# Performance work log

Measured on AMD Instinct MI355X. Metric: run time of the kernel, lower is better.

## Reference

```python
import math
import jax, jax.numpy as jnp
import numpy as np

EMBED_DIM = 512
MAX_LEN = 5000
BATCH = 16
SEQ = 4096


def _make_pe(max_len, embed_dim):
    pos = jnp.arange(max_len, dtype=jnp.float32)[:, None]
    div = jnp.exp(jnp.arange(0, embed_dim, 2, dtype=jnp.float32) * (-math.log(10000.0) / embed_dim))
    pe = jnp.zeros((max_len, embed_dim), dtype=jnp.float32)
    pe = pe.at[:, 0::2].set(jnp.sin(pos * div))
    pe = pe.at[:, 1::2].set(jnp.cos(pos * div))
    return pe[None]  # [1, max_len, embed_dim]


def setup_inputs() -> dict:
    key = jax.random.key(0)
    k1, k2 = jax.random.split(key)
    x = jax.random.normal(k1, (BATCH, SEQ, EMBED_DIM), dtype=jnp.float32)
    pe = _make_pe(MAX_LEN, EMBED_DIM)
    # RZ angles: present in the original module but provably do not affect
    # the PauliZ expectations (diagonal phases + basis-permuting CNOTs).
    param = jax.random.normal(k2, (EMBED_DIM,), dtype=jnp.float32)
    quantum_weight = jnp.full((1,), 0.5, dtype=jnp.float32)
    return {"x": x, "pe": pe, "param": param, "quantum_weight": quantum_weight}


def reference(x, pe, param, quantum_weight):
    # out = x + positional encoding
    out = x + pe[:, : x.shape[1]]  # [B, S, D]
    # Closed form of the RY(out_i)->RZ(param_i)->CNOT-chain circuit:
    #   b'_i = XOR(b_0..b_i)  =>  <Z_i> = prod_{j<=i} cos(out_j)
    # (RZ phases cancel in computational-basis probabilities; param unused.)
    quantum_out = jnp.cumprod(jnp.cos(out), axis=-1)  # [B, S, D]
    w = jax.nn.sigmoid(quantum_weight[0])
    return w * quantum_out + (1.0 - w) * out
```

## Files before the change

kernel.cpp:

```cpp
#include <hip/hip_runtime.h>

constexpr int D = 512;
constexpr int S = 4096;
constexpr int B = 16;
constexpr int ROWS = B * S;
constexpr int WAVES_PER_BLOCK = 4;

__global__ __launch_bounds__(256) void qpe_kernel(
    const float* __restrict__ x, const float* __restrict__ pe,
    const float* __restrict__ qw, float* __restrict__ out)
{
    const int lane = threadIdx.x & 63;
    const int wid  = threadIdx.x >> 6;
    const int row  = blockIdx.x * WAVES_PER_BLOCK + wid;
    const int s    = row & (S - 1);

    const float w   = 1.0f / (1.0f + __expf(-qw[0]));
    const float omw = 1.0f - w;

    const size_t base = (size_t)row * D + (size_t)lane * 8;
    const float4* xp = (const float4*)(x + base);
    const float4* pp = (const float4*)(pe + (size_t)s * D + (size_t)lane * 8);

    const float4 x0 = xp[0], x1 = xp[1];
    const float4 p0 = pp[0], p1 = pp[1];

    float o[8] = { x0.x + p0.x, x0.y + p0.y, x0.z + p0.z, x0.w + p0.w,
                   x1.x + p1.x, x1.y + p1.y, x1.z + p1.z, x1.w + p1.w };

    float c[8];
    #pragma unroll
    for (int j = 0; j < 8; ++j) c[j] = __cosf(o[j]);

    float p = c[0];
    #pragma unroll
    for (int j = 1; j < 8; ++j) p *= c[j];

    #pragma unroll
    for (int off = 1; off < 64; off <<= 1) {
        float n = __shfl_up(p, off, 64);
        if (lane >= off) p *= n;
    }
    float prefix = __shfl_up(p, 1, 64);
    if (lane == 0) prefix = 1.0f;

    float run = prefix;
    float r[8];
    #pragma unroll
    for (int j = 0; j < 8; ++j) {
        run *= c[j];
        r[j] = w * run + omw * o[j];
    }

    float4* op = (float4*)(out + base);
    op[0] = make_float4(r[0], r[1], r[2], r[3]);
    op[1] = make_float4(r[4], r[5], r[6], r[7]);
}

extern "C" void kernel_launch(void* const* d_in, const int* in_sizes, int n_in,
                              void* d_out, int out_size, void* d_ws, size_t ws_size,
                              hipStream_t stream) {
    const float* x  = (const float*)d_in[0];
    const float* pe = (const float*)d_in[1];
    const float* qw = (const float*)d_in[3];
    float* out = (float*)d_out;

    const int blocks = ROWS / WAVES_PER_BLOCK;
    qpe_kernel<<<blocks, WAVES_PER_BLOCK * 64, 0, stream>>>(x, pe, qw, out);
}
```

Baseline: 55.71 us.

## Use DPP wave scan, process two rows per wave, nontemporal stores

Replaces the shuffle-based multiplicative prefix scan with DPP row_shr and row_bcast instructions, which avoids LDS-backed permutes. Each wave now handles two rows so more loads are in flight per wave, and the grid is halved. Output is written with nontemporal stores to reduce cache pollution. The kernel is memory bound, so gains depend on latency hiding and write behavior.

```diff
diff --git a/kernel.cpp b/kernel.cpp
--- a/kernel.cpp
+++ b/kernel.cpp
@@ -5,66 +5,103 @@
 constexpr int B = 16;
 constexpr int ROWS = B * S;
 constexpr int WAVES_PER_BLOCK = 4;
+constexpr int ROWS_PER_WAVE  = 2;
+
+typedef float fx4 __attribute__((ext_vector_type(4)));
+
+template<int CTRL, int ROW_MASK>
+__device__ __forceinline__ float dpp_mul(float x) {
+    int t = __builtin_amdgcn_update_dpp(0x3f800000, __float_as_int(x),
+                                        CTRL, ROW_MASK, 0xF, false);
+    return x * __int_as_float(t);
+}
+
+__device__ __forceinline__ float wave_incl_mul_scan(float p) {
+    p = dpp_mul<0x111, 0xF>(p);
+    p = dpp_mul<0x112, 0xF>(p);
+    p = dpp_mul<0x114, 0xF>(p);
+    p = dpp_mul<0x118, 0xF>(p);
+    p = dpp_mul<0x142, 0xA>(p);
+    p = dpp_mul<0x143, 0xC>(p);
+    return p;
+}
+
+__device__ __forceinline__ float wave_shr1_id(float p) {
+    int t = __builtin_amdgcn_update_dpp(0x3f800000, __float_as_int(p),
+                                        0x138 , 0xF, 0xF, false);
+    return __int_as_float(t);
+}
 
 __global__ __launch_bounds__(256) void qpe_kernel(
-    const float* __restrict__ x, const float* __restrict__ pe,
-    const float* __restrict__ qw, float* __restrict__ out)
+    const fx4* __restrict__ x4, const fx4* __restrict__ pe4,
+    const float* __restrict__ qw, fx4* __restrict__ out4)
 {
     const int lane = threadIdx.x & 63;
     const int wid  = threadIdx.x >> 6;
-    const int row  = blockIdx.x * WAVES_PER_BLOCK + wid;
-    const int s    = row & (S - 1);
+    const int wave = blockIdx.x * WAVES_PER_BLOCK + wid;
+    const int row0 = wave * ROWS_PER_WAVE;
 
     const float w   = 1.0f / (1.0f + __expf(-qw[0]));
     const float omw = 1.0f - w;
 
-    const size_t base = (size_t)row * D + (size_t)lane * 8;
-    const float4* xp = (const float4*)(x + base);
-    const float4* pp = (const float4*)(pe + (size_t)s * D + (size_t)lane * 8);
+    fx4 xv[2][2], pv[2][2];
+    size_t xb[2];
+    #pragma unroll
+    for (int r = 0; r < ROWS_PER_WAVE; ++r) {
+        const int row = row0 + r;
+        const int s   = row & (S - 1);
+        xb[r] = (size_t)row * (D / 4) + (size_t)lane * 2;
+        const size_t pb = (size_t)s * (D / 4) + (size_t)lane * 2;
+        xv[r][0] = x4[xb[r]];     xv[r][1] = x4[xb[r] + 1];
+        pv[r][0] = pe4[pb];       pv[r][1] = pe4[pb + 1];
+    }
 
-    const float4 x0 = xp[0], x1 = xp[1];
-    const float4 p0 = pp[0], p1 = pp[1];
-
-    float o[8] = { x0.x + p0.x, x0.y + p0.y, x0.z + p0.z, x0.w + p0.w,
-                   x1.x + p1.x, x1.y + p1.y, x1.z + p1.z, x1.w + p1.w };
-
-    float c[8];
+    float o[2][8], c[2][8], p[2];
     #pragma unroll
-    for (int j = 0; j < 8; ++j) c[j] = __cosf(o[j]);
-
-    float p = c[0];
-    #pragma unroll
-    for (int j = 1; j < 8; ++j) p *= c[j];
+    for (int r = 0; r < ROWS_PER_WAVE; ++r) {
+        #pragma unroll
+        for (int j = 0; j < 4; ++j) {
+            o[r][j]     = xv[r][0][j] + pv[r][0][j];
+            o[r][4 + j] = xv[r][1][j] + pv[r][1][j];
+        }
+        #pragma unroll
+        for (int j = 0; j < 8; ++j) c[r][j] = __cosf(o[r][j]);
+        float q = c[r][0];
+        #pragma unroll
+        for (int j = 1; j < 8; ++j) q *= c[r][j];
+        p[r] = q;
+    }
 
     #pragma unroll
-    for (int off = 1; off < 64; off <<= 1) {
-        float n = __shfl_up(p, off, 64);
-        if (lane >= off) p *= n;
-    }
-    float prefix = __shfl_up(p, 1, 64);
-    if (lane == 0) prefix = 1.0f;
-
-    float run = prefix;
-    float r[8];
-    #pragma unroll
-    for (int j = 0; j < 8; ++j) {
-        run *= c[j];
-        r[j] = w * run + omw * o[j];
+    for (int r = 0; r < ROWS_PER_WAVE; ++r) {
+        p[r] = wave_incl_mul_scan(p[r]);
+        p[r] = wave_shr1_id(p[r]);
     }
 
-    float4* op = (float4*)(out + base);
-    op[0] = make_float4(r[0], r[1], r[2], r[3]);
-    op[1] = make_float4(r[4], r[5], r[6], r[7]);
+    #pragma unroll
+    for (int r = 0; r < ROWS_PER_WAVE; ++r) {
+        float run = p[r];
+        float res[8];
+        #pragma unroll
+        for (int j = 0; j < 8; ++j) {
+            run *= c[r][j];
+            res[j] = w * run + omw * o[r][j];
+        }
+        fx4 s0 = { res[0], res[1], res[2], res[3] };
+        fx4 s1 = { res[4], res[5], res[6], res[7] };
+        __builtin_nontemporal_store(s0, &out4[xb[r]]);
+        __builtin_nontemporal_store(s1, &out4[xb[r] + 1]);
+    }
 }
 
 extern "C" void kernel_launch(void* const* d_in, const int* in_sizes, int n_in,
                               void* d_out, int out_size, void* d_ws, size_t ws_size,
                               hipStream_t stream) {
-    const float* x  = (const float*)d_in[0];
-    const float* pe = (const float*)d_in[1];
-    const float* qw = (const float*)d_in[3];
-    float* out = (float*)d_out;
+    const fx4* x  = (const fx4*)d_in[0];
+    const fx4* pe = (const fx4*)d_in[1];
+    const float* qw  = (const float*)d_in[3];
+    fx4* out = (fx4*)d_out;
 
-    const int blocks = ROWS / WAVES_PER_BLOCK;
+    const int blocks = ROWS / (WAVES_PER_BLOCK * ROWS_PER_WAVE);
     qpe_kernel<<<blocks, WAVES_PER_BLOCK * 64, 0, stream>>>(x, pe, qw, out);
 }
```

Result: no change. 55.11 us (-1.1%).
